# Performance work log

Hardware: AMD Instinct MI355X
Metric: run time of the kernel (lower is better)

The kernel has to match this reference:

```python
import jax, jax.numpy as jnp
import numpy as np

B, T, N_EMBED, HEAD_SIZE = 8, 2048, 1024, 64


def setup_inputs() -> dict:
    key = jax.random.key(0)
    k1, k2, k3, k4 = jax.random.split(key, 4)
    x = jax.random.normal(k1, (B, T, N_EMBED), dtype=jnp.float32)
    # nn.Linear(n_embed, head_size, bias=False): y = x @ W^T; store as [in, out]
    s = 1.0 / np.sqrt(N_EMBED)
    Wk = jax.random.normal(k2, (N_EMBED, HEAD_SIZE), dtype=jnp.float32) * s
    Wq = jax.random.normal(k3, (N_EMBED, HEAD_SIZE), dtype=jnp.float32) * s
    Wv = jax.random.normal(k4, (N_EMBED, HEAD_SIZE), dtype=jnp.float32) * s
    return {"x": x, "Wk": Wk, "Wq": Wq, "Wv": Wv}


def reference(x, Wk, Wq, Wv):
    batch, time, embed = x.shape
    k = x @ Wk  # [B,T,H]
    q = x @ Wq
    v = x @ Wv
    # NOTE: original scales by input embed size (not head_size)
    wei = jnp.einsum('bth,bsh->bts', q, k) * (embed ** -0.5)  # [B,T(query),T(key)]
    tril = jnp.tril(jnp.ones((time, time), dtype=bool))
    wei = jnp.where(tril[None, :, :], wei, -jnp.inf)
    # NOTE: original applies softmax over dim=1 (query axis), not the last axis
    p = jax.nn.softmax(wei, axis=1)
    return jnp.einsum('bts,bsh->bth', p, v)
```

## Files before the change

kernel.cpp:

```cpp
#include <hip/hip_runtime.h>
#include <hip/hip_bf16.h>

typedef __attribute__((ext_vector_type(8))) short short8;
typedef __attribute__((ext_vector_type(4))) float f32x4;

#define B_  8
#define T_  2048
#define E_  1024
#define H_  64
#define SCALE 0.03125f

__device__ inline unsigned short f2bf(float f) {
    unsigned int u = __builtin_bit_cast(unsigned int, f);
    unsigned int r = (u + 0x7FFFu + ((u >> 16) & 1u)) >> 16;
    return (unsigned short)r;
}
__device__ inline unsigned int packbf(float lo, float hi) {
    return (unsigned int)f2bf(lo) | ((unsigned int)f2bf(hi) << 16);
}
__device__ inline void glds16(const void* g, void* l) {
    __builtin_amdgcn_global_load_lds((const __attribute__((address_space(1))) void*)g,
                                     (__attribute__((address_space(3))) void*)l, 16, 0, 0);
}

__global__ __launch_bounds__(256) void prep_w(const float* __restrict__ Wq,
                                              const float* __restrict__ Wk,
                                              const float* __restrict__ Wv,
                                              unsigned short* __restrict__ Wt) {
    __shared__ float ls[64][65];
    int tid = threadIdx.x;
    int wsel = blockIdx.x >> 4, kt = blockIdx.x & 15;
    const float* W = (wsel == 0) ? Wq : (wsel == 1) ? Wk : Wv;
    int kr = tid >> 2, c4 = (tid & 3) * 16;
    const float* src = W + (long)(kt * 64 + kr) * H_ + c4;
    #pragma unroll
    for (int i = 0; i < 4; ++i) {
        float4 v = *(const float4*)(src + 4 * i);
        ls[kr][c4 + 4 * i + 0] = v.x; ls[kr][c4 + 4 * i + 1] = v.y;
        ls[kr][c4 + 4 * i + 2] = v.z; ls[kr][c4 + 4 * i + 3] = v.w;
    }
    __syncthreads();
    int c = tid >> 2, kk = (tid & 3) * 16;
    unsigned short* dst = Wt + (long)(wsel * 64 + c) * E_ + kt * 64 + kk;
    uint4 o1, o2;
    o1.x = packbf(ls[kk + 0][c], ls[kk + 1][c]);  o1.y = packbf(ls[kk + 2][c], ls[kk + 3][c]);
    o1.z = packbf(ls[kk + 4][c], ls[kk + 5][c]);  o1.w = packbf(ls[kk + 6][c], ls[kk + 7][c]);
    o2.x = packbf(ls[kk + 8][c], ls[kk + 9][c]);  o2.y = packbf(ls[kk + 10][c], ls[kk + 11][c]);
    o2.z = packbf(ls[kk + 12][c], ls[kk + 13][c]);o2.w = packbf(ls[kk + 14][c], ls[kk + 15][c]);
    *(uint4*)dst = o1;
    *(uint4*)(dst + 8) = o2;
}

__global__ __launch_bounds__(512, 4) void qkv_gemm(const float* __restrict__ x,
                                                   const unsigned short* __restrict__ Wt,
                                                   unsigned short* __restrict__ qb,
                                                   unsigned short* __restrict__ kb,
                                                   unsigned short* __restrict__ vt) {
    __shared__ unsigned short wlds[2][192 * 64];
    __shared__ unsigned short xlds[2][32 * 72];

    int tid = threadIdx.x, lane = tid & 63, w = tid >> 6;
    int l15 = lane & 15, lg = lane >> 4;
    int wr = w & 1, wc = w >> 1;
    int r0 = blockIdx.x * 32;
    int b = r0 >> 11, tb = r0 & 2047;

    int l8 = lane >> 3, s8 = lane & 7;
    int swz = s8 ^ l8;
    const unsigned short* wg = Wt + (long)(24 * w + l8) * E_ + swz * 8;
    unsigned short* wl0 = &wlds[0][(24 * w) * 64];
    unsigned short* wl1 = &wlds[1][(24 * w) * 64];

    int xr = tid >> 4, xcf = (tid & 15) * 4;
    const float* xg = x + (long)(r0 + xr) * E_ + xcf;

    f32x4 acc[3];
    #pragma unroll
    for (int i = 0; i < 3; ++i) acc[i] = (f32x4){0.f, 0.f, 0.f, 0.f};

    {
        float4 xa = *(const float4*)xg;
        #pragma unroll
        for (int j = 0; j < 3; ++j)
            glds16(wg + (long)(8 * j) * E_, wl0 + (8 * j) * 64);
        uint2 ua; ua.x = packbf(xa.x, xa.y); ua.y = packbf(xa.z, xa.w);
        *(uint2*)&xlds[0][xr * 72 + xcf] = ua;
    }

    for (int ks = 0; ks < 16; ++ks) {
        int cur = ks & 1;
        __builtin_amdgcn_s_barrier();
        __builtin_amdgcn_sched_barrier(0);
        float4 xa;
        if (ks < 15) {
            int kp = (ks + 1) * 64;
            xa = *(const float4*)(xg + kp);
            unsigned short* wldst = cur ? wl0 : wl1;
            #pragma unroll
            for (int j = 0; j < 3; ++j)
                glds16(wg + (long)(8 * j) * E_ + kp, wldst + (8 * j) * 64);
            asm volatile("s_waitcnt vmcnt(4) lgkmcnt(0)" ::: "memory");
        } else {
            asm volatile("s_waitcnt vmcnt(0) lgkmcnt(0)" ::: "memory");
        }
        __builtin_amdgcn_sched_barrier(0);
        __builtin_amdgcn_s_barrier();
        __builtin_amdgcn_sched_barrier(0);

        const char* wb = (const char*)&wlds[cur][0];
        const char* xsb = (const char*)&xlds[cur][0];
        #pragma unroll
        for (int kk2 = 0; kk2 < 2; ++kk2) {
            short8 a = *(const short8*)(xsb + (16 * wr + l15) * 144 + kk2 * 64 + lg * 16);
            #pragma unroll
            for (int ct = 0; ct < 3; ++ct) {
                int c = 48 * wc + 16 * ct + l15;
                int sp = (kk2 * 4 + lg) ^ (c & 7);
                short8 bf = *(const short8*)(wb + c * 128 + sp * 16);
                acc[ct] = __builtin_amdgcn_mfma_f32_16x16x32_bf16(a, bf, acc[ct], 0, 0, 0);
            }
        }
        if (ks < 15) {
            uint2 ua; ua.x = packbf(xa.x, xa.y); ua.y = packbf(xa.z, xa.w);
            *(uint2*)&xlds[cur ^ 1][xr * 72 + xcf] = ua;
        }
    }

    #pragma unroll
    for (int ct = 0; ct < 3; ++ct) {
        int col = 48 * wc + 16 * ct + l15;
        if (col < 128) {
            unsigned short* dst = (col < 64) ? qb : kb;
            int n = col & 63;
            #pragma unroll
            for (int r = 0; r < 4; ++r) {
                int t = tb + 16 * wr + lg * 4 + r;
                dst[((long)b * T_ + t) * H_ + n] = f2bf(acc[ct][r]);
            }
        }
    }
    float* vbuf = (float*)&wlds[0][0];
    #pragma unroll
    for (int ct = 0; ct < 3; ++ct) {
        int col = 48 * wc + 16 * ct + l15;
        if (col >= 128) {
            int h = col - 128;
            #pragma unroll
            for (int r = 0; r < 4; ++r)
                vbuf[(16 * wr + lg * 4 + r) * 68 + h] = acc[ct][r];
        }
    }
    __syncthreads();
    {
        int h = tid >> 3, tc = (tid & 7) * 4;
        uint2 o;
        o.x = packbf(vbuf[(tc + 0) * 68 + h], vbuf[(tc + 1) * 68 + h]);
        o.y = packbf(vbuf[(tc + 2) * 68 + h], vbuf[(tc + 3) * 68 + h]);
        *(uint2*)&vt[((long)b * H_ + h) * T_ + tb + tc] = o;
    }
}

__global__ __launch_bounds__(256) void col_partial(const unsigned short* __restrict__ qb,
                                                   const unsigned short* __restrict__ kb,
                                                   float* __restrict__ colD) {
    __shared__ unsigned short qlds[2][64 * 64];
    int tid = threadIdx.x, lane = tid & 63, w = tid >> 6;
    int l15 = lane & 15, lg = lane >> 4;
    int bid = blockIdx.x;
    int p = bid & 3, j = (bid >> 2) & 31, b = bid >> 7;
    int sb = 64 * j + 16 * w;

    const unsigned short* kp = kb + ((long)b * T_ + sb + l15) * H_;
    short8 bk0 = *(const short8*)(kp + lg * 8);
    short8 bk1 = *(const short8*)(kp + 32 + lg * 8);

    int l8 = lane >> 3, s8 = lane & 7;
    int swz8 = (s8 ^ l8) * 8;
    const unsigned short* qg = qb + ((long)b * T_ + w * 16 + l8) * H_ + swz8;
    unsigned short* qd0 = &qlds[0][w * 16 * 64];
    unsigned short* qd1 = &qlds[1][w * 16 * 64];

    float d = 0.f;
    int first = 64 * j + 64 * p;
    int m = (first < T_) ? ((T_ - first + 255) >> 8) : 0;

    if (m > 0) {
        glds16(qg + (long)first * H_, qd0);
        glds16(qg + (long)first * H_ + 8 * H_, qd0 + 8 * 64);
    }

    for (int i = 0; i < m; ++i) {
        int cur = i & 1;
        __builtin_amdgcn_s_barrier();
        __builtin_amdgcn_sched_barrier(0);
        if (i + 1 < m) {
            long tn = first + 256 * (i + 1);
            unsigned short* qd = cur ? qd0 : qd1;
            glds16(qg + tn * H_, qd);
            glds16(qg + tn * H_ + 8 * H_, qd + 8 * 64);
            asm volatile("s_waitcnt vmcnt(2)" ::: "memory");
        } else {
            asm volatile("s_waitcnt vmcnt(0)" ::: "memory");
        }
        __builtin_amdgcn_sched_barrier(0);
        __builtin_amdgcn_s_barrier();
        __builtin_amdgcn_sched_barrier(0);

        int t_base = first + 256 * i;
        const unsigned short* qt = &qlds[cur][0];
        bool diag = (t_base == 64 * j);
        #pragma unroll
        for (int st = 0; st < 4; ++st) {
            if (diag && st < w) continue;
            int trow = 16 * st + l15;
            short8 a0 = *(const short8*)&qt[trow * 64 + ((0 + lg) ^ (trow & 7)) * 8];
            short8 a1 = *(const short8*)&qt[trow * 64 + ((4 + lg) ^ (trow & 7)) * 8];
            f32x4 acc = (f32x4){0.f, 0.f, 0.f, 0.f};
            acc = __builtin_amdgcn_mfma_f32_16x16x32_bf16(a0, bk0, acc, 0, 0, 0);
            acc = __builtin_amdgcn_mfma_f32_16x16x32_bf16(a1, bk1, acc, 0, 0, 0);
            if (diag && st == w) {
                #pragma unroll
                for (int r = 0; r < 4; ++r) {
                    float e = __expf(acc[r] * SCALE);
                    if ((16 * st + lg * 4 + r) < (16 * w + l15)) e = 0.f;
                    d += e;
                }
            } else {
                #pragma unroll
                for (int r = 0; r < 4; ++r)
                    d += __expf(acc[r] * SCALE);
            }
        }
    }
    d += __shfl_xor(d, 16, 64);
    d += __shfl_xor(d, 32, 64);
    if (lane < 16)
        colD[(long)p * (B_ * T_) + (long)b * T_ + sb + lane] = d;
}

__global__ __launch_bounds__(256) void finalize(const float* __restrict__ colD,
                                                float* __restrict__ colR,
                                                float* __restrict__ out) {
    int tid = threadIdx.x;
    long bid = blockIdx.x;
    uint4 z = (uint4){0u, 0u, 0u, 0u};
    *(uint4*)(out + (bid * 256 + tid) * 4) = z;
    if (bid < 64) {
        int i = (int)bid * 256 + tid;
        float s = colD[i] + colD[B_ * T_ + i] + colD[2 * B_ * T_ + i] + colD[3 * B_ * T_ + i];
        colR[i] = 1.0f / s;
    }
}

__global__ __launch_bounds__(256, 4) void attn_out(const unsigned short* __restrict__ qb,
                                                   const unsigned short* __restrict__ kb,
                                                   const unsigned short* __restrict__ vt,
                                                   const float* __restrict__ colR,
                                                   float* __restrict__ out) {
    __shared__ unsigned short kv[2][8192];
    __shared__ unsigned short pbuf[4][16 * 40];

    int tid = threadIdx.x, lane = tid & 63, w = tid >> 6;
    int qw = w & 1, sw = w >> 1;
    int l15 = lane & 15, lg = lane >> 4;
    int idx = blockIdx.x;
    int p = idx & 1;
    int b = (idx >> 1) & 7;
    int j = 63 - (idx >> 4);
    int t0 = j * 32;

    const unsigned short* kbase = kb + (long)b * T_ * H_;
    const unsigned short* vbase = vt + (long)b * H_ * T_;
    const float* cR = colR + b * T_;

    const unsigned short* qp = qb + ((long)b * T_ + t0 + qw * 16 + l15) * H_ + lg * 8;
    short8 qa0 = *(const short8*)qp;
    short8 qa1 = *(const short8*)(qp + 32);

    int l8 = lane >> 3, s8 = lane & 7;
    int swz8 = (s8 ^ l8) * 8;
    const unsigned short* kg = kbase + (long)(w * 16 + l8) * H_ + swz8;
    const unsigned short* vg = vbase + (long)(w * 16 + l8) * T_ + swz8;
    unsigned short* kd0 = &kv[0][w * 16 * 64];
    unsigned short* vd0 = &kv[0][4096 + w * 16 * 64];
    unsigned short* kd1 = &kv[1][w * 16 * 64];
    unsigned short* vd1 = &kv[1][4096 + w * 16 * 64];

    f32x4 o[4];
    #pragma unroll
    for (int i = 0; i < 4; ++i) o[i] = (f32x4){0.f, 0.f, 0.f, 0.f};
    unsigned short* myp = pbuf[w];

    int nstt = j / 2 + 1;
    int m = (nstt - p + 1) >> 1;
    int off = (m > 0) ? (j % m) : 0;

    if (m > 0) {
        int s0 = (p + 2 * off) * 64;
        glds16(kg + (long)s0 * H_, kd0);  glds16(kg + (long)s0 * H_ + 8 * H_, kd0 + 8 * 64);
        glds16(vg + s0, vd0);             glds16(vg + s0 + 8 * T_, vd0 + 8 * 64);
    }

    for (int i = 0; i < m; ++i) {
        int cur = i & 1;
        __builtin_amdgcn_s_barrier();
        __builtin_amdgcn_sched_barrier(0);
        if (i + 1 < m) {
            int rot = i + 1 + off; if (rot >= m) rot -= m;
            int sn = (p + 2 * rot) * 64;
            unsigned short* kd = cur ? kd0 : kd1;
            unsigned short* vd = cur ? vd0 : vd1;
            glds16(kg + (long)sn * H_, kd);
            glds16(kg + (long)sn * H_ + 8 * H_, kd + 8 * 64);
            glds16(vg + sn, vd);
            glds16(vg + sn + 8 * T_, vd + 8 * 64);
            asm volatile("s_waitcnt vmcnt(4)" ::: "memory");
        } else {
            asm volatile("s_waitcnt vmcnt(0)" ::: "memory");
        }
        __builtin_amdgcn_sched_barrier(0);
        __builtin_amdgcn_s_barrier();
        __builtin_amdgcn_sched_barrier(0);

        int rotc = i + off; if (rotc >= m) rotc -= m;
        int s0 = (p + 2 * rotc) * 64;
        const unsigned short* kt = &kv[cur][0];
        const unsigned short* vtl = &kv[cur][4096];

        #pragma unroll
        for (int ct = 0; ct < 2; ++ct) {
            int row = sw * 32 + ct * 16 + l15;
            short8 k0 = *(const short8*)&kt[row * 64 + ((0 + lg) ^ (row & 7)) * 8];
            short8 k1 = *(const short8*)&kt[row * 64 + ((4 + lg) ^ (row & 7)) * 8];
            f32x4 acc = (f32x4){0.f, 0.f, 0.f, 0.f};
            acc = __builtin_amdgcn_mfma_f32_16x16x32_bf16(qa0, k0, acc, 0, 0, 0);
            acc = __builtin_amdgcn_mfma_f32_16x16x32_bf16(qa1, k1, acc, 0, 0, 0);
            int s = s0 + row;
            float rr = cR[s];
            #pragma unroll
            for (int r = 0; r < 4; ++r) {
                int t = t0 + qw * 16 + lg * 4 + r;
                float pv = __expf(acc[r] * SCALE) * rr;
                if (s > t) pv = 0.f;
                myp[(lg * 4 + r) * 40 + ct * 16 + l15] = f2bf(pv);
            }
        }
        short8 pa = *(const short8*)&myp[l15 * 40 + lg * 8];
        #pragma unroll
        for (int ht = 0; ht < 4; ++ht) {
            int vrow = ht * 16 + l15;
            short8 vf = *(const short8*)&vtl[vrow * 64 + ((sw * 4 + lg) ^ (vrow & 7)) * 8];
            o[ht] = __builtin_amdgcn_mfma_f32_16x16x32_bf16(pa, vf, o[ht], 0, 0, 0);
        }
    }

    __syncthreads();
    float* rbuf = (float*)&kv[0][0];
    if (sw == 1) {
        #pragma unroll
        for (int ht = 0; ht < 4; ++ht)
            #pragma unroll
            for (int r = 0; r < 4; ++r)
                rbuf[(qw * 16 + lg * 4 + r) * 68 + ht * 16 + l15] = o[ht][r];
    }
    __syncthreads();
    if (sw == 0) {
        float* ob = out + ((long)b * T_ + t0 + qw * 16) * H_;
        #pragma unroll
        for (int ht = 0; ht < 4; ++ht)
            #pragma unroll
            for (int r = 0; r < 4; ++r) {
                int rr_ = lg * 4 + r, cc = ht * 16 + l15;
                unsafeAtomicAdd(&ob[(long)rr_ * H_ + cc],
                                o[ht][r] + rbuf[(qw * 16 + rr_) * 68 + cc]);
            }
    }
}

extern "C" void kernel_launch(void* const* d_in, const int* in_sizes, int n_in,
                              void* d_out, int out_size, void* d_ws, size_t ws_size,
                              hipStream_t stream) {
    const float* x  = (const float*)d_in[0];
    const float* Wk = (const float*)d_in[1];
    const float* Wq = (const float*)d_in[2];
    const float* Wv = (const float*)d_in[3];
    float* out = (float*)d_out;

    char* ws = (char*)d_ws;
    unsigned short* Wt = (unsigned short*)ws;
    unsigned short* qb = (unsigned short*)(ws + 393216);
    unsigned short* kb = (unsigned short*)(ws + 393216 + 2097152);
    unsigned short* vt = (unsigned short*)(ws + 393216 + 2 * 2097152);
    float* colR = (float*)(ws + 393216 + 3 * 2097152);
    float* colD = colR + B_ * T_;

    prep_w     <<<48,   256, 0, stream>>>(Wq, Wk, Wv, Wt);
    qkv_gemm   <<<512,  512, 0, stream>>>(x, Wt, qb, kb, vt);
    col_partial<<<1024, 256, 0, stream>>>(qb, kb, colD);
    finalize   <<<1024, 256, 0, stream>>>(colD, colR, out);
    attn_out   <<<1024, 256, 0, stream>>>(qb, kb, vt, colR, out);
}
```

Baseline: 58.63 us.

## Triple-buffer LDS prefetch in col_partial and attn_out for two-ahead loads

Both the column-denominator kernel and the attention output kernel move from double to triple buffering of Q and K/V tiles in LDS. Loads are now issued two iterations ahead, with waitcnt thresholds adjusted to match, to hide more global-memory latency. attn_out's launch-bounds occupancy hint drops from 4 to 2 blocks per SIMD to allow for the larger LDS footprint. The cost is more LDS per block and possibly fewer resident waves to hide latency.

```diff
diff --git a/kernel.cpp b/kernel.cpp
--- a/kernel.cpp
+++ b/kernel.cpp
@@ -163,7 +163,7 @@
 __global__ __launch_bounds__(256) void col_partial(const unsigned short* __restrict__ qb,
                                                    const unsigned short* __restrict__ kb,
                                                    float* __restrict__ colD) {
-    __shared__ unsigned short qlds[2][64 * 64];
+    __shared__ unsigned short qlds[3][64 * 64];
     int tid = threadIdx.x, lane = tid & 63, w = tid >> 6;
     int l15 = lane & 15, lg = lane >> 4;
     int bid = blockIdx.x;
@@ -177,27 +177,33 @@
     int l8 = lane >> 3, s8 = lane & 7;
     int swz8 = (s8 ^ l8) * 8;
     const unsigned short* qg = qb + ((long)b * T_ + w * 16 + l8) * H_ + swz8;
-    unsigned short* qd0 = &qlds[0][w * 16 * 64];
-    unsigned short* qd1 = &qlds[1][w * 16 * 64];
 
     float d = 0.f;
     int first = 64 * j + 64 * p;
     int m = (first < T_) ? ((T_ - first + 255) >> 8) : 0;
 
     if (m > 0) {
-        glds16(qg + (long)first * H_, qd0);
-        glds16(qg + (long)first * H_ + 8 * H_, qd0 + 8 * 64);
+        unsigned short* qd = &qlds[0][w * 16 * 64];
+        glds16(qg + (long)first * H_, qd);
+        glds16(qg + (long)first * H_ + 8 * H_, qd + 8 * 64);
+    }
+    if (m > 1) {
+        long t1 = first + 256;
+        unsigned short* qd = &qlds[1][w * 16 * 64];
+        glds16(qg + t1 * H_, qd);
+        glds16(qg + t1 * H_ + 8 * H_, qd + 8 * 64);
     }
 
     for (int i = 0; i < m; ++i) {
-        int cur = i & 1;
-        __builtin_amdgcn_s_barrier();
-        __builtin_amdgcn_sched_barrier(0);
-        if (i + 1 < m) {
-            long tn = first + 256 * (i + 1);
-            unsigned short* qd = cur ? qd0 : qd1;
+        __builtin_amdgcn_s_barrier();
+        __builtin_amdgcn_sched_barrier(0);
+        if (i + 2 < m) {
+            long tn = first + 256 * (i + 2);
+            unsigned short* qd = &qlds[(i + 2) % 3][w * 16 * 64];
             glds16(qg + tn * H_, qd);
             glds16(qg + tn * H_ + 8 * H_, qd + 8 * 64);
+            asm volatile("s_waitcnt vmcnt(4)" ::: "memory");
+        } else if (i + 1 < m) {
             asm volatile("s_waitcnt vmcnt(2)" ::: "memory");
         } else {
             asm volatile("s_waitcnt vmcnt(0)" ::: "memory");
@@ -207,7 +213,7 @@
         __builtin_amdgcn_sched_barrier(0);
 
         int t_base = first + 256 * i;
-        const unsigned short* qt = &qlds[cur][0];
+        const unsigned short* qt = &qlds[i % 3][0];
         bool diag = (t_base == 64 * j);
         #pragma unroll
         for (int st = 0; st < 4; ++st) {
@@ -252,12 +258,12 @@
     }
 }
 
-__global__ __launch_bounds__(256, 4) void attn_out(const unsigned short* __restrict__ qb,
+__global__ __launch_bounds__(256, 2) void attn_out(const unsigned short* __restrict__ qb,
                                                    const unsigned short* __restrict__ kb,
                                                    const unsigned short* __restrict__ vt,
                                                    const float* __restrict__ colR,
                                                    float* __restrict__ out) {
-    __shared__ unsigned short kv[2][8192];
+    __shared__ unsigned short kv[3][8192];
     __shared__ unsigned short pbuf[4][16 * 40];
 
     int tid = threadIdx.x, lane = tid & 63, w = tid >> 6;
@@ -281,10 +287,6 @@
     int swz8 = (s8 ^ l8) * 8;
     const unsigned short* kg = kbase + (long)(w * 16 + l8) * H_ + swz8;
     const unsigned short* vg = vbase + (long)(w * 16 + l8) * T_ + swz8;
-    unsigned short* kd0 = &kv[0][w * 16 * 64];
-    unsigned short* vd0 = &kv[0][4096 + w * 16 * 64];
-    unsigned short* kd1 = &kv[1][w * 16 * 64];
-    unsigned short* vd1 = &kv[1][4096 + w * 16 * 64];
 
     f32x4 o[4];
     #pragma unroll
@@ -296,24 +298,36 @@
     int off = (m > 0) ? (j % m) : 0;
 
     if (m > 0) {
-        int s0 = (p + 2 * off) * 64;
-        glds16(kg + (long)s0 * H_, kd0);  glds16(kg + (long)s0 * H_ + 8 * H_, kd0 + 8 * 64);
-        glds16(vg + s0, vd0);             glds16(vg + s0 + 8 * T_, vd0 + 8 * 64);
+        int r0i = off;
+        int s0 = (p + 2 * r0i) * 64;
+        unsigned short* kd = &kv[0][w * 16 * 64];
+        unsigned short* vd = &kv[0][4096 + w * 16 * 64];
+        glds16(kg + (long)s0 * H_, kd);  glds16(kg + (long)s0 * H_ + 8 * H_, kd + 8 * 64);
+        glds16(vg + s0, vd);             glds16(vg + s0 + 8 * T_, vd + 8 * 64);
+    }
+    if (m > 1) {
+        int r1i = 1 + off; if (r1i >= m) r1i -= m;
+        int s1 = (p + 2 * r1i) * 64;
+        unsigned short* kd = &kv[1][w * 16 * 64];
+        unsigned short* vd = &kv[1][4096 + w * 16 * 64];
+        glds16(kg + (long)s1 * H_, kd);  glds16(kg + (long)s1 * H_ + 8 * H_, kd + 8 * 64);
+        glds16(vg + s1, vd);             glds16(vg + s1 + 8 * T_, vd + 8 * 64);
     }
 
     for (int i = 0; i < m; ++i) {
-        int cur = i & 1;
-        __builtin_amdgcn_s_barrier();
-        __builtin_amdgcn_sched_barrier(0);
-        if (i + 1 < m) {
-            int rot = i + 1 + off; if (rot >= m) rot -= m;
+        __builtin_amdgcn_s_barrier();
+        __builtin_amdgcn_sched_barrier(0);
+        if (i + 2 < m) {
+            int rot = i + 2 + off; while (rot >= m) rot -= m;
             int sn = (p + 2 * rot) * 64;
-            unsigned short* kd = cur ? kd0 : kd1;
-            unsigned short* vd = cur ? vd0 : vd1;
+            unsigned short* kd = &kv[(i + 2) % 3][w * 16 * 64];
+            unsigned short* vd = &kv[(i + 2) % 3][4096 + w * 16 * 64];
             glds16(kg + (long)sn * H_, kd);
             glds16(kg + (long)sn * H_ + 8 * H_, kd + 8 * 64);
             glds16(vg + sn, vd);
             glds16(vg + sn + 8 * T_, vd + 8 * 64);
+            asm volatile("s_waitcnt vmcnt(8)" ::: "memory");
+        } else if (i + 1 < m) {
             asm volatile("s_waitcnt vmcnt(4)" ::: "memory");
         } else {
             asm volatile("s_waitcnt vmcnt(0)" ::: "memory");
@@ -322,10 +336,10 @@
         __builtin_amdgcn_s_barrier();
         __builtin_amdgcn_sched_barrier(0);
 
-        int rotc = i + off; if (rotc >= m) rotc -= m;
+        int rotc = i + off; while (rotc >= m) rotc -= m;
         int s0 = (p + 2 * rotc) * 64;
-        const unsigned short* kt = &kv[cur][0];
-        const unsigned short* vtl = &kv[cur][4096];
+        const unsigned short* kt = &kv[i % 3][0];
+        const unsigned short* vtl = &kv[i % 3][4096];
 
         #pragma unroll
         for (int ct = 0; ct < 2; ++ct) {
```

Result: slower. 60.62 us (+3.4%).
